# Kernel tuning notes

Hardware: AMD Instinct MI355X
Metric: run time of the kernel (lower is better)

Reference implementation:

```python
import jax, jax.numpy as jnp
import numpy as np

L, U, D_IN, D_OUT, B = 6, 256, 784, 10, 32768  # num_layers, units, input_dim, output_dim, batch


def setup_inputs() -> dict:
    key = jax.random.key(0)
    ks = jax.random.split(key, 7)
    s = jnp.float32(0.05)  # keras 'random_normal' initializer stddev
    return {
        "x": jax.random.normal(ks[0], (B, D_IN), jnp.float32),
        "W_in": jax.random.normal(ks[1], (D_IN, U), jnp.float32) * s,
        "b_in": jax.random.normal(ks[2], (U,), jnp.float32) * s,
        "B0": jax.random.normal(ks[3], (L, U, U), jnp.float32) * s,   # per-layer B0
        "q": jax.random.normal(ks[4], (L, U), jnp.float32) * s,       # per-layer q
        "W_out": jax.random.normal(ks[5], (U, D_OUT), jnp.float32) * s,
        "b_out": jax.random.normal(ks[6], (D_OUT,), jnp.float32) * s,
    }


def reference(x, W_in, b_in, B0, q, W_out, b_out):
    u = W_in.shape[1]
    v0 = (x @ W_in + b_in).T          # (u, B)
    v1 = jnp.tanh(v0)                  # activation of layer 0 applied once before the loop

    def step(carry, params):
        v0, v1 = carry
        B0_l, q_l = params
        z = jnp.zeros((u, u), B0_l.dtype)
        # skew-symmetric block system [[0, B0], [-B0^T, 0]]
        A = jnp.block([[z, B0_l], [-B0_l.T, z]])           # (2u, 2u)
        rhs = jnp.concatenate([v0 + q_l[:, None], v1], 0)   # (2u, B)
        sol = jnp.linalg.solve(A, rhs)
        return (sol[:u], sol[u:]), None

    (v0, v1), _ = jax.lax.scan(step, (v0, v1), (B0, q))
    return v0.T @ W_out + b_out        # (B, D_OUT)
```

## Files before the change

### kernel.cpp

```cpp
#include <hip/hip_runtime.h>
#include <math.h>

#define NU      256
#define NLAYERS 6
#define NBATCH  32768
#define NDIN    784
#define NDOUT   10
#define NUSQ    65536

typedef unsigned short u16;
typedef __attribute__((ext_vector_type(8))) short s16x8;
typedef __attribute__((ext_vector_type(4))) float f32x4;

__device__ __forceinline__ u16 f2bf(float x) {
    union { float f; unsigned u; } a; a.f = x;
    const unsigned r = a.u + 0x7fffu + ((a.u >> 16) & 1u);
    return (u16)(r >> 16);
}
__device__ __forceinline__ float bf2f(u16 h) {
    union { unsigned u; float f; } a; a.u = ((unsigned)h) << 16; return a.f;
}

__device__ __forceinline__ void gl_lds16(const u16* g, u16* l) {
    __builtin_amdgcn_global_load_lds(
        (const __attribute__((address_space(1))) void*)g,
        (__attribute__((address_space(3))) void*)l, 16, 0, 0);
}

#define COL_CASES(BODY) \
    case 0:  BODY(0);  break; case 1:  BODY(1);  break; \
    case 2:  BODY(2);  break; case 3:  BODY(3);  break; \
    case 4:  BODY(4);  break; case 5:  BODY(5);  break; \
    case 6:  BODY(6);  break; case 7:  BODY(7);  break; \
    case 8:  BODY(8);  break; case 9:  BODY(9);  break; \
    case 10: BODY(10); break; case 11: BODY(11); break; \
    case 12: BODY(12); break; case 13: BODY(13); break; \
    case 14: BODY(14); break; case 15: BODY(15); break; \
    case 16: BODY(16); break; case 17: BODY(17); break; \
    case 18: BODY(18); break; case 19: BODY(19); break; \
    case 20: BODY(20); break; case 21: BODY(21); break; \
    case 22: BODY(22); break; case 23: BODY(23); break; \
    case 24: BODY(24); break; case 25: BODY(25); break; \
    case 26: BODY(26); break; case 27: BODY(27); break; \
    case 28: BODY(28); break; case 29: BODY(29); break; \
    case 30: BODY(30); break; case 31: BODY(31); break;

__global__ __launch_bounds__(512, 2) void fused_inv_ingemm(
    const float* __restrict__ B0, const float* __restrict__ qg,
    u16* __restrict__ wnnh, u16* __restrict__ wnnl,
    u16* __restrict__ wnth, u16* __restrict__ wntl,
    float* __restrict__ bq,
    const float* __restrict__ X, const float* __restrict__ Win,
    const float* __restrict__ bin,
    u16* __restrict__ V0h, u16* __restrict__ V0l,
    u16* __restrict__ V1h, u16* __restrict__ V1l)
{
    __shared__ __align__(16) float colv[2][256];
    __shared__ int   s_p[2];
    __shared__ float s_pv[2];
    __shared__ int   pivrow[256];
    __shared__ int   ilogrow[256];
    __shared__ float qs[256];
    __shared__ float part[8][256];
    __shared__ __align__(16) float As[16][128];
    __shared__ __align__(16) float Bs[16][128];

    const int tid = threadIdx.x;

    if (blockIdx.x < NLAYERS) {
        const int layer = blockIdx.x;
        const int ct = tid & 63;
        const int wv = tid >> 6;

        float a[32][4];
        const float* Ablk = B0 + (size_t)layer * NU * NU;
#pragma unroll
        for (int j = 0; j < 4; ++j) {
            const float* rp = Ablk + (size_t)(ct*4 + j)*NU + wv*32;
#pragma unroll
            for (int i = 0; i < 32; i += 4) {
                const float4 v = *(const float4*)(rp + i);
                a[i+0][j] = v.x; a[i+1][j] = v.y; a[i+2][j] = v.z; a[i+3][j] = v.w;
            }
        }

        int used = 0;

        for (int k = 0; k < 256; ++k) {
            const int wvk = k >> 5, ikk = k & 31, buf = k & 1;

            if (wv == wvk) {
                float c0, c1, c2, c3;
#define EXT(I) { c0 = a[I][0]; c1 = a[I][1]; c2 = a[I][2]; c3 = a[I][3]; }
                switch (ikk) { COL_CASES(EXT) }
#undef EXT
                float ba = -1.0f, bv = 1.0f; int br = 0;
                {
                    float av;
                    av = (used & 1) ? -1.0f : fabsf(c0);
                    if (av > ba) { ba = av; bv = c0; br = ct*4 + 0; }
                    av = (used & 2) ? -1.0f : fabsf(c1);
                    if (av > ba) { ba = av; bv = c1; br = ct*4 + 1; }
                    av = (used & 4) ? -1.0f : fabsf(c2);
                    if (av > ba) { ba = av; bv = c2; br = ct*4 + 2; }
                    av = (used & 8) ? -1.0f : fabsf(c3);
                    if (av > ba) { ba = av; bv = c3; br = ct*4 + 3; }
                }
#pragma unroll
                for (int off = 32; off > 0; off >>= 1) {
                    const float oa = __shfl_down(ba, off);
                    const float ov = __shfl_down(bv, off);
                    const int   orr = __shfl_down(br, off);
                    if (oa > ba) { ba = oa; bv = ov; br = orr; }
                }
                float4 cw; cw.x = c0; cw.y = c1; cw.z = c2; cw.w = c3;
                *(float4*)(&colv[buf][ct*4]) = cw;
                if (ct == 0) {
                    s_p[buf] = br;
                    s_pv[buf] = 1.0f / bv;
                    pivrow[k] = br;
                }
            }
            __syncthreads();

            const int   p      = __builtin_amdgcn_readfirstlane(s_p[buf]);
            const float pivinv = s_pv[buf];
            const int ctp = p >> 2, jp = p & 3;

            const float4 dv = *(const float4*)(&colv[buf][ct*4]);

            float t[32];
#define SEL(J) { _Pragma("unroll") for (int i = 0; i < 32; ++i) t[i] = a[i][J]; }
            switch (jp) {
                case 0: SEL(0) break; case 1: SEL(1) break;
                case 2: SEL(2) break; default: SEL(3) break;
            }
#undef SEL
            float prw[32];
#pragma unroll
            for (int i = 0; i < 32; ++i) prw[i] = __shfl(t[i], ctp) * pivinv;

            if (wv == wvk) {
#define ZCOL(I) { prw[I] = pivinv; a[I][0] = 0.0f; a[I][1] = 0.0f; a[I][2] = 0.0f; a[I][3] = 0.0f; }
                switch (ikk) { COL_CASES(ZCOL) }
#undef ZCOL
            }

            const float d0 = -dv.x, d1 = -dv.y, d2 = -dv.z, d3 = -dv.w;
#pragma unroll
            for (int i = 0; i < 32; ++i) {
                const float pw = prw[i];
                a[i][0] = fmaf(d0, pw, a[i][0]);
                a[i][1] = fmaf(d1, pw, a[i][1]);
                a[i][2] = fmaf(d2, pw, a[i][2]);
                a[i][3] = fmaf(d3, pw, a[i][3]);
            }

            const bool mine = (ct == ctp);
#define OWR(J) { _Pragma("unroll") for (int i = 0; i < 32; ++i) a[i][J] = mine ? prw[i] : a[i][J]; }
            switch (jp) {
                case 0: OWR(0) break; case 1: OWR(1) break;
                case 2: OWR(2) break; default: OWR(3) break;
            }
#undef OWR
            if (mine) used |= (1 << jp);
        }
        __syncthreads();

        if (tid < 256) { ilogrow[pivrow[tid]] = tid; qs[tid] = qg[(size_t)layer*NU + tid]; }
        __syncthreads();

        {
            float s0=0.f, s1=0.f, s2=0.f, s3=0.f;
#pragma unroll
            for (int i = 0; i < 32; ++i) {
                const float qq = qs[pivrow[wv*32 + i]];
                s0 = fmaf(a[i][0], qq, s0);
                s1 = fmaf(a[i][1], qq, s1);
                s2 = fmaf(a[i][2], qq, s2);
                s3 = fmaf(a[i][3], qq, s3);
            }
            part[wv][ct*4+0] = s0; part[wv][ct*4+1] = s1;
            part[wv][ct*4+2] = s2; part[wv][ct*4+3] = s3;
        }
        __syncthreads();
        if (tid < 256) {
            float s = 0.f;
#pragma unroll
            for (int w2 = 0; w2 < 8; ++w2) s += part[w2][tid];
            bq[(size_t)layer*NU + ilogrow[tid]] = s;
        }

        u16* nh = wnnh + (size_t)layer*NUSQ; u16* nl = wnnl + (size_t)layer*NUSQ;
        u16* th = wnth + (size_t)layer*NUSQ; u16* tl = wntl + (size_t)layer*NUSQ;
#pragma unroll
        for (int j = 0; j < 4; ++j) {
            const int r = ilogrow[ct*4 + j];
#pragma unroll
            for (int i = 0; i < 32; ++i) {
                const int c = pivrow[wv*32 + i];
                const float v = a[i][j];
                const u16 h  = f2bf(v);
                const u16 lo = f2bf(v - bf2f(h));
                th[(size_t)r*NU + c] = h;  tl[(size_t)r*NU + c] = lo;
                nh[(size_t)c*NU + r] = h;  nl[(size_t)c*NU + r] = lo;
            }
        }
        return;
    }

    if (tid >= 256) return;

    const int bid = blockIdx.x - NLAYERS;
    const int m0 = (bid & 255) * 128;
    const int n0 = (bid >> 8) * 128;
    const int t  = tid;
    const int tx = t & 15, ty = t >> 4;
    const int K = NDIN;

    float acc[8][8];
#pragma unroll
    for (int i = 0; i < 8; ++i)
#pragma unroll
        for (int j = 0; j < 8; ++j) acc[i][j] = 0.0f;

    const int am = t >> 1;
    const int ak = (t & 1) * 8;
    const int bk = t >> 4;
    const int bn = (t & 15) * 8;

    for (int k0 = 0; k0 < K; k0 += 16) {
        const float* Ap = X + (size_t)(m0 + am)*K + (k0 + ak);
        const float4 a0 = *(const float4*)(Ap);
        const float4 a1 = *(const float4*)(Ap + 4);
        As[ak+0][am] = a0.x; As[ak+1][am] = a0.y; As[ak+2][am] = a0.z; As[ak+3][am] = a0.w;
        As[ak+4][am] = a1.x; As[ak+5][am] = a1.y; As[ak+6][am] = a1.z; As[ak+7][am] = a1.w;
        const float* Bp = Win + (size_t)(k0 + bk)*NU + (n0 + bn);
        const float4 b0 = *(const float4*)(Bp);
        const float4 b1 = *(const float4*)(Bp + 4);
        *(float4*)(&Bs[bk][bn])   = b0;
        *(float4*)(&Bs[bk][bn+4]) = b1;
        __syncthreads();
#pragma unroll
        for (int kk = 0; kk < 16; ++kk) {
            float af[8], bf[8];
            *(float4*)(af)   = *(const float4*)(&As[kk][ty*8]);
            *(float4*)(af+4) = *(const float4*)(&As[kk][ty*8+4]);
            *(float4*)(bf)   = *(const float4*)(&Bs[kk][tx*8]);
            *(float4*)(bf+4) = *(const float4*)(&Bs[kk][tx*8+4]);
#pragma unroll
            for (int i = 0; i < 8; ++i)
#pragma unroll
                for (int j = 0; j < 8; ++j)
                    acc[i][j] = fmaf(af[i], bf[j], acc[i][j]);
        }
        __syncthreads();
    }

#pragma unroll
    for (int i = 0; i < 8; ++i) {
        const size_t row = m0 + ty*8 + i;
        s16x8 vh, vl, th2, tl2;
#pragma unroll
        for (int j = 0; j < 8; ++j) {
            const float v = acc[i][j] + bin[n0 + tx*8 + j];
            const u16 h  = f2bf(v);
            vh[j] = (short)h; vl[j] = (short)f2bf(v - bf2f(h));
            const float tv = tanhf(v);
            const u16 h2 = f2bf(tv);
            th2[j] = (short)h2; tl2[j] = (short)f2bf(tv - bf2f(h2));
        }
        const size_t o = row*NU + n0 + tx*8;
        *(s16x8*)&V0h[o] = vh; *(s16x8*)&V0l[o] = vl;
        *(s16x8*)&V1h[o] = th2; *(s16x8*)&V1l[o] = tl2;
    }
}

__global__ __launch_bounds__(256, 2) void gemm_mfma(
    const u16* __restrict__ Ah, const u16* __restrict__ Al,
    const u16* __restrict__ Bh, const u16* __restrict__ Bl,
    u16* __restrict__ Ch, u16* __restrict__ Cl,
    const float* __restrict__ bias, const float alpha)
{
    __shared__ __align__(16) u16 lAh[128*32], lAl[128*32], lBh[128*32], lBl[128*32];
    const int t    = threadIdx.x;
    const int lane = t & 63;
    const int w    = t >> 6;
    const int wr = w >> 1, wc = w & 1;
    const int qd = lane >> 4, l15 = lane & 15;
    const int m0 = blockIdx.x * 128, n0 = blockIdx.y * 128;

    const int srow = t >> 2;
    const int skc  = (t & 3) * 8;

    f32x4 acc[4][4];
    const f32x4 z = {0.f, 0.f, 0.f, 0.f};
#pragma unroll
    for (int i = 0; i < 4; ++i)
#pragma unroll
        for (int j = 0; j < 4; ++j) acc[i][j] = z;

    for (int k0 = 0; k0 < NU; k0 += 32) {
#pragma unroll
        for (int half = 0; half < 2; ++half) {
            const int rr = srow + half*64;
            const size_t ga = (size_t)(m0 + rr)*NU + k0 + skc;
            const size_t gb = (size_t)(n0 + rr)*NU + k0 + skc;
            const int lo = rr*32 + skc;
            gl_lds16(Ah + ga, &lAh[lo]);
            gl_lds16(Al + ga, &lAl[lo]);
            gl_lds16(Bh + gb, &lBh[lo]);
            gl_lds16(Bl + gb, &lBl[lo]);
        }
        __syncthreads();

        s16x8 ah[4], al[4], bh[4], bl[4];
#pragma unroll
        for (int mt = 0; mt < 4; ++mt) {
            const int off = (wr*64 + mt*16 + l15)*32 + qd*8;
            ah[mt] = *(const s16x8*)&lAh[off];
            al[mt] = *(const s16x8*)&lAl[off];
        }
#pragma unroll
        for (int nt = 0; nt < 4; ++nt) {
            const int off = (wc*64 + nt*16 + l15)*32 + qd*8;
            bh[nt] = *(const s16x8*)&lBh[off];
            bl[nt] = *(const s16x8*)&lBl[off];
        }
#pragma unroll
        for (int mt = 0; mt < 4; ++mt)
#pragma unroll
            for (int nt = 0; nt < 4; ++nt) {
                acc[mt][nt] = __builtin_amdgcn_mfma_f32_16x16x32_bf16(ah[mt], bh[nt], acc[mt][nt], 0, 0, 0);
                acc[mt][nt] = __builtin_amdgcn_mfma_f32_16x16x32_bf16(ah[mt], bl[nt], acc[mt][nt], 0, 0, 0);
                acc[mt][nt] = __builtin_amdgcn_mfma_f32_16x16x32_bf16(al[mt], bh[nt], acc[mt][nt], 0, 0, 0);
            }
        __syncthreads();
    }

#pragma unroll
    for (int mt = 0; mt < 4; ++mt) {
#pragma unroll
        for (int nt = 0; nt < 4; ++nt) {
            const int col = n0 + wc*64 + nt*16 + l15;
            const float bb = bias ? bias[col] : 0.0f;
#pragma unroll
            for (int r = 0; r < 4; ++r) {
                const int row = m0 + wr*64 + mt*16 + qd*4 + r;
                const float v = alpha*acc[mt][nt][r] + bb;
                const u16 h  = f2bf(v);
                const u16 lo = f2bf(v - bf2f(h));
                const size_t o = (size_t)row*NU + col;
                Ch[o] = h; Cl[o] = lo;
            }
        }
    }
}

__global__ __launch_bounds__(256) void out_gemm(
    const u16* __restrict__ V0h, const u16* __restrict__ V0l,
    const float* __restrict__ Wout,
    const float* __restrict__ bout, float* __restrict__ out)
{
    __shared__ float Ws[NU*NDOUT];
    const int t = threadIdx.x;
    for (int i = t; i < NU*NDOUT; i += 256) Ws[i] = Wout[i];
    __syncthreads();
    const int lane = t & 63;
    const int wv = t >> 6;
    const int row = blockIdx.x*4 + wv;
    float acc[NDOUT];
#pragma unroll
    for (int j = 0; j < NDOUT; ++j) acc[j] = 0.0f;
#pragma unroll
    for (int s = 0; s < 4; ++s) {
        const int k = lane + 64*s;
        const size_t o = (size_t)row*NU + k;
        const float v = bf2f(V0h[o]) + bf2f(V0l[o]);
#pragma unroll
        for (int j = 0; j < NDOUT; ++j) acc[j] = fmaf(v, Ws[k*NDOUT + j], acc[j]);
    }
#pragma unroll
    for (int off = 32; off > 0; off >>= 1) {
#pragma unroll
        for (int j = 0; j < NDOUT; ++j) acc[j] += __shfl_down(acc[j], off);
    }
    if (lane == 0) {
#pragma unroll
        for (int j = 0; j < NDOUT; ++j) out[(size_t)row*NDOUT + j] = acc[j] + bout[j];
    }
}

extern "C" void kernel_launch(void* const* d_in, const int* in_sizes, int n_in,
                              void* d_out, int out_size, void* d_ws, size_t ws_size,
                              hipStream_t stream)
{
    const float* x    = (const float*)d_in[0];
    const float* Win  = (const float*)d_in[1];
    const float* bin  = (const float*)d_in[2];
    const float* B0   = (const float*)d_in[3];
    const float* q    = (const float*)d_in[4];
    const float* Wout = (const float*)d_in[5];
    const float* bout = (const float*)d_in[6];
    float* out = (float*)d_out;

    u16* wnnh = (u16*)d_ws;
    u16* wnnl = wnnh + (size_t)NLAYERS*NUSQ;
    u16* wnth = wnnl + (size_t)NLAYERS*NUSQ;
    u16* wntl = wnth + (size_t)NLAYERS*NUSQ;
    float* bq = (float*)(wntl + (size_t)NLAYERS*NUSQ);
    u16* pl   = (u16*)(bq + NLAYERS*NU);
    const size_t PSZ = (size_t)NBATCH*NU;
    u16* sAh = pl;           u16* sAl = sAh + PSZ;
    u16* sBh = sAl + PSZ;    u16* sBl = sBh + PSZ;
    u16* sCh = sBl + PSZ;    u16* sCl = sCh + PSZ;

    fused_inv_ingemm<<<NLAYERS + 512, 512, 0, stream>>>(
        B0, q, wnnh, wnnl, wnth, wntl, bq,
        x, Win, bin, sAh, sAl, sBh, sBl);

    const dim3 ggrid(NBATCH/128, NU/128);

    u16 *v0h = sAh, *v0l = sAl, *v1h = sBh, *v1l = sBl, *frh = sCh, *frl = sCl;
    for (int l = 0; l < NLAYERS; ++l) {
        const size_t wo = (size_t)l*NUSQ;
        gemm_mfma<<<ggrid, 256, 0, stream>>>(v1h, v1l, wnnh + wo, wnnl + wo,
                                             frh, frl, nullptr, -1.0f);
        gemm_mfma<<<ggrid, 256, 0, stream>>>(v0h, v0l, wnth + wo, wntl + wo,
                                             v1h, v1l, bq + (size_t)l*NU, 1.0f);
        u16* t0 = v0h; u16* t1 = v0l;
        v0h = frh; v0l = frl; frh = t0; frl = t1;
    }
    out_gemm<<<NBATCH/4, 256, 0, stream>>>(v0h, v0l, Wout, bout, out);
}
```

Before: 1.016 ms.

## Share X tile across both column halves and fuse Gauss-Jordan elimination with readlane

The input GEMM now uses all 512 threads per block: each half computes one 128-column output half while sharing a single staged X tile. This halves the grid and removes the redundant global reads of X that two separate blocks used to make. The in-kernel matrix inversion replaces the select, shuffle, update and overwrite passes with a single loop that broadcasts the pivot row through readlane and writes the updated values in place. This trades idle threads and extra memory traffic for higher register and LDS use per block.

```diff
diff --git a/kernel.cpp b/kernel.cpp
--- a/kernel.cpp
+++ b/kernel.cpp
@@ -19,6 +19,9 @@
 }
 __device__ __forceinline__ float bf2f(u16 h) {
     union { unsigned u; float f; } a; a.u = ((unsigned)h) << 16; return a.f;
+}
+__device__ __forceinline__ float rdlane(float v, int lane) {
+    return __uint_as_float(__builtin_amdgcn_readlane(__float_as_uint(v), lane));
 }
 
 __device__ __forceinline__ void gl_lds16(const u16* g, u16* l) {
@@ -63,7 +66,7 @@
     __shared__ float qs[256];
     __shared__ float part[8][256];
     __shared__ __align__(16) float As[16][128];
-    __shared__ __align__(16) float Bs[16][128];
+    __shared__ __align__(16) float Bs[2][16][128];
 
     const int tid = threadIdx.x;
 
@@ -126,43 +129,37 @@
             const int   p      = __builtin_amdgcn_readfirstlane(s_p[buf]);
             const float pivinv = s_pv[buf];
             const int ctp = p >> 2, jp = p & 3;
+            const bool mine = (ct == ctp);
 
             const float4 dv = *(const float4*)(&colv[buf][ct*4]);
-
-            float t[32];
-#define SEL(J) { _Pragma("unroll") for (int i = 0; i < 32; ++i) t[i] = a[i][J]; }
+            const float e0 = -dv.x, e1 = -dv.y, e2 = -dv.z, e3 = -dv.w;
+
+#define ELIM(JP) { _Pragma("unroll") for (int i = 0; i < 32; ++i) { \
+                const float c  = rdlane(a[i][JP], ctp); \
+                const float pv = c * pivinv; \
+                const float r0 = fmaf(e0, pv, a[i][0]); \
+                const float r1 = fmaf(e1, pv, a[i][1]); \
+                const float r2 = fmaf(e2, pv, a[i][2]); \
+                const float r3 = fmaf(e3, pv, a[i][3]); \
+                a[i][0] = (mine && JP == 0) ? pv : r0; \
+                a[i][1] = (mine && JP == 1) ? pv : r1; \
+                a[i][2] = (mine && JP == 2) ? pv : r2; \
+                a[i][3] = (mine && JP == 3) ? pv : r3; } }
             switch (jp) {
-                case 0: SEL(0) break; case 1: SEL(1) break;
-                case 2: SEL(2) break; default: SEL(3) break;
-            }
-#undef SEL
-            float prw[32];
-#pragma unroll
-            for (int i = 0; i < 32; ++i) prw[i] = __shfl(t[i], ctp) * pivinv;
+                case 0: ELIM(0) break; case 1: ELIM(1) break;
+                case 2: ELIM(2) break; default: ELIM(3) break;
+            }
+#undef ELIM
 
             if (wv == wvk) {
-#define ZCOL(I) { prw[I] = pivinv; a[I][0] = 0.0f; a[I][1] = 0.0f; a[I][2] = 0.0f; a[I][3] = 0.0f; }
-                switch (ikk) { COL_CASES(ZCOL) }
-#undef ZCOL
-            }
-
-            const float d0 = -dv.x, d1 = -dv.y, d2 = -dv.z, d3 = -dv.w;
-#pragma unroll
-            for (int i = 0; i < 32; ++i) {
-                const float pw = prw[i];
-                a[i][0] = fmaf(d0, pw, a[i][0]);
-                a[i][1] = fmaf(d1, pw, a[i][1]);
-                a[i][2] = fmaf(d2, pw, a[i][2]);
-                a[i][3] = fmaf(d3, pw, a[i][3]);
-            }
-
-            const bool mine = (ct == ctp);
-#define OWR(J) { _Pragma("unroll") for (int i = 0; i < 32; ++i) a[i][J] = mine ? prw[i] : a[i][J]; }
-            switch (jp) {
-                case 0: OWR(0) break; case 1: OWR(1) break;
-                case 2: OWR(2) break; default: OWR(3) break;
-            }
-#undef OWR
+#define ZFIX(I) { \
+                a[I][0] = (mine && jp == 0) ? pivinv : e0 * pivinv; \
+                a[I][1] = (mine && jp == 1) ? pivinv : e1 * pivinv; \
+                a[I][2] = (mine && jp == 2) ? pivinv : e2 * pivinv; \
+                a[I][3] = (mine && jp == 3) ? pivinv : e3 * pivinv; }
+                switch (ikk) { COL_CASES(ZFIX) }
+#undef ZFIX
+            }
             if (mine) used |= (1 << jp);
         }
         __syncthreads();
@@ -209,13 +206,12 @@
         return;
     }
 
-    if (tid >= 256) return;
-
-    const int bid = blockIdx.x - NLAYERS;
-    const int m0 = (bid & 255) * 128;
-    const int n0 = (bid >> 8) * 128;
-    const int t  = tid;
-    const int tx = t & 15, ty = t >> 4;
+    const int bid  = blockIdx.x - NLAYERS;
+    const int m0   = bid * 128;
+    const int half = tid >> 8;
+    const int t2   = tid & 255;
+    const int n0   = half * 128;
+    const int tx = t2 & 15, ty = t2 >> 4;
     const int K = NDIN;
 
     float acc[8][8];
@@ -224,30 +220,34 @@
 #pragma unroll
         for (int j = 0; j < 8; ++j) acc[i][j] = 0.0f;
 
-    const int am = t >> 1;
-    const int ak = (t & 1) * 8;
-    const int bk = t >> 4;
-    const int bn = (t & 15) * 8;
+    const int am = t2 >> 1;
+    const int ak = (t2 & 1) * 8;
+    const int bk = t2 >> 4;
+    const int bn = (t2 & 15) * 8;
 
     for (int k0 = 0; k0 < K; k0 += 16) {
-        const float* Ap = X + (size_t)(m0 + am)*K + (k0 + ak);
-        const float4 a0 = *(const float4*)(Ap);
-        const float4 a1 = *(const float4*)(Ap + 4);
-        As[ak+0][am] = a0.x; As[ak+1][am] = a0.y; As[ak+2][am] = a0.z; As[ak+3][am] = a0.w;
-        As[ak+4][am] = a1.x; As[ak+5][am] = a1.y; As[ak+6][am] = a1.z; As[ak+7][am] = a1.w;
-        const float* Bp = Win + (size_t)(k0 + bk)*NU + (n0 + bn);
-        const float4 b0 = *(const float4*)(Bp);
-        const float4 b1 = *(const float4*)(Bp + 4);
-        *(float4*)(&Bs[bk][bn])   = b0;
-        *(float4*)(&Bs[bk][bn+4]) = b1;
+        if (half == 0) {
+            const float* Ap = X + (size_t)(m0 + am)*K + (k0 + ak);
+            const float4 a0 = *(const float4*)(Ap);
+            const float4 a1 = *(const float4*)(Ap + 4);
+            As[ak+0][am] = a0.x; As[ak+1][am] = a0.y; As[ak+2][am] = a0.z; As[ak+3][am] = a0.w;
+            As[ak+4][am] = a1.x; As[ak+5][am] = a1.y; As[ak+6][am] = a1.z; As[ak+7][am] = a1.w;
+        }
+        {
+            const float* Bp = Win + (size_t)(k0 + bk)*NU + (n0 + bn);
+            const float4 b0 = *(const float4*)(Bp);
+            const float4 b1 = *(const float4*)(Bp + 4);
+            *(float4*)(&Bs[half][bk][bn])   = b0;
+            *(float4*)(&Bs[half][bk][bn+4]) = b1;
+        }
         __syncthreads();
 #pragma unroll
         for (int kk = 0; kk < 16; ++kk) {
             float af[8], bf[8];
             *(float4*)(af)   = *(const float4*)(&As[kk][ty*8]);
             *(float4*)(af+4) = *(const float4*)(&As[kk][ty*8+4]);
-            *(float4*)(bf)   = *(const float4*)(&Bs[kk][tx*8]);
-            *(float4*)(bf+4) = *(const float4*)(&Bs[kk][tx*8+4]);
+            *(float4*)(bf)   = *(const float4*)(&Bs[half][kk][tx*8]);
+            *(float4*)(bf+4) = *(const float4*)(&Bs[half][kk][tx*8+4]);
 #pragma unroll
             for (int i = 0; i < 8; ++i)
 #pragma unroll
@@ -271,7 +271,7 @@
             th2[j] = (short)h2; tl2[j] = (short)f2bf(tv - bf2f(h2));
         }
         const size_t o = row*NU + n0 + tx*8;
-        *(s16x8*)&V0h[o] = vh; *(s16x8*)&V0l[o] = vl;
+        *(s16x8*)&V0h[o] = vh;  *(s16x8*)&V0l[o] = vl;
         *(s16x8*)&V1h[o] = th2; *(s16x8*)&V1l[o] = tl2;
     }
 }
@@ -415,7 +415,7 @@
     u16* sBh = sAl + PSZ;    u16* sBl = sBh + PSZ;
     u16* sCh = sBl + PSZ;    u16* sCl = sCh + PSZ;
 
-    fused_inv_ingemm<<<NLAYERS + 512, 512, 0, stream>>>(
+    fused_inv_ingemm<<<NLAYERS + 256, 512, 0, stream>>>(
         B0, q, wnnh, wnnl, wnth, wntl, bq,
         x, Win, bin, sAh, sAl, sBh, sBl);
 
```

New measurement: 1.429 ms. 40.7% more time.
